# Performance work log

Hardware: AMD Instinct MI355X
Metric: run time of the kernel (lower is better)

The kernel has to match this reference:

```python
import jax, jax.numpy as jnp
import numpy as np
from jax import lax

DIM = 256
HEADS = 8
SR = 4
EPS = 1e-5
SCALE = (DIM // HEADS) ** -0.5


def _dwconv(x, wgt, stride, pad):
    # x: (B,C,H,W), wgt: (C,1,kh,kw) depthwise
    return lax.conv_general_dilated(
        x, wgt, (stride, stride), [(pad, pad), (pad, pad)],
        feature_group_count=x.shape[1],
        dimension_numbers=("NCHW", "OIHW", "NCHW"))


def _bn(x, g, b, m, v):
    # eval-mode batchnorm folded to per-channel scale/shift
    s = g / jnp.sqrt(v + EPS)
    return x * s[:, None, None] + (b - m * s)[:, None, None]


def setup_inputs() -> dict:
    key = jax.random.key(0)
    ks = jax.random.split(key, 16)
    b, h, w = 8, 64, 64
    c = DIM
    n = h * w

    def rn(k, shape, s=0.05):
        return jax.random.normal(k, shape, jnp.float32) * s

    return dict(
        x=jax.random.normal(ks[0], (b, n, c), jnp.float32),
        h=h, w=w,
        Wq=rn(ks[1], (c, c)), bq=rn(ks[2], (c,)),
        Wkv=rn(ks[3], (2 * c, c)), bkv=rn(ks[4], (2 * c,)),
        sr_w1=rn(ks[5], (c, 1, SR + 3, SR + 3), 0.1),
        bn1_gamma=1.0 + rn(ks[6], (c,)), bn1_beta=rn(ks[7], (c,)),
        bn1_mean=rn(ks[8], (c,)), bn1_var=jnp.abs(1.0 + rn(ks[9], (c,))),
        sr_w2=1.0 + rn(ks[10], (c,), 0.2),  # 1x1 depthwise conv == per-channel scale
        bn2_gamma=1.0 + rn(ks[11], (c,)), bn2_beta=rn(ks[12], (c,)),
        bn2_mean=rn(ks[13], (c,)), bn2_var=jnp.abs(1.0 + rn(ks[14], (c,))),
        local_w=rn(ks[15], (c, 1, 3, 3), 0.1),
        local_b=jnp.zeros((c,), jnp.float32),
    )


def reference(x, h, w, Wq, bq, Wkv, bkv, sr_w1, bn1_gamma, bn1_beta, bn1_mean,
              bn1_var, sr_w2, bn2_gamma, bn2_beta, bn2_mean, bn2_var,
              local_w, local_b):
    b, n, c = x.shape
    hd = c // HEADS
    xi = x.transpose(0, 2, 1).reshape(b, c, h, w)  # (b,c,h,w)

    # q projection (1x1 conv == channel matmul)
    q = jnp.einsum("bchw,dc->bdhw", xi, Wq) + bq[None, :, None, None]
    q = q.reshape(b, HEADS, hd, n).transpose(0, 1, 3, 2)  # (b,H,n,hd)

    # spatial reduction: dwconv7 s4 + BN + GELU + dw1x1 + BN
    kv = _dwconv(xi, sr_w1, SR, (SR + 3) // 2)
    kv = _bn(kv, bn1_gamma, bn1_beta, bn1_mean, bn1_var)
    kv = jax.nn.gelu(kv, approximate=False)
    kv = kv * sr_w2[None, :, None, None]
    kv = _bn(kv, bn2_gamma, bn2_beta, bn2_mean, bn2_var)

    # residual local depthwise 3x3 conv
    kv = _dwconv(kv, local_w, 1, 1) + local_b[None, :, None, None] + kv

    # kv projection and split
    kvp = jnp.einsum("bchw,dc->bdhw", kv, Wkv) + bkv[None, :, None, None]
    k_, v_ = jnp.split(kvp, 2, axis=1)
    m = k_.shape[2] * k_.shape[3]
    k_ = k_.reshape(b, HEADS, hd, m)                       # (b,H,hd,m)
    v_ = v_.reshape(b, HEADS, hd, m).transpose(0, 1, 3, 2)  # (b,H,m,hd)

    attn = jax.nn.softmax(jnp.einsum("bhnd,bhdm->bhnm", q, k_) * SCALE, axis=-1)
    out = jnp.einsum("bhnm,bhmd->bhnd", attn, v_)           # (b,H,n,hd)
    out = out.transpose(0, 1, 3, 2).reshape(b, c, n).transpose(0, 2, 1)
    return out
```

## Files before the change

kernel.cpp:

```cpp
#include <hip/hip_runtime.h>
#include <math.h>

typedef __bf16 bf16;
typedef bf16 bf16x4 __attribute__((ext_vector_type(4)));
typedef bf16 bf16x8 __attribute__((ext_vector_type(8)));
typedef float f32x4 __attribute__((ext_vector_type(4)));

static_assert(sizeof(bf16x8) == 16, "bf16x8 must be 16B");

#define QSCALE (0.17677669529663687f * 1.4426950408889634f)

__device__ __forceinline__ f32x4 mfma16(bf16x8 a, bf16x8 b, f32x4 c) {
  return __builtin_amdgcn_mfma_f32_16x16x32_bf16(a, b, c, 0, 0, 0);
}

__global__ __launch_bounds__(256) void k_cvt(
    const float* __restrict__ Wq, const float* __restrict__ Wkv,
    const float* __restrict__ w7, bf16* __restrict__ Wqb,
    bf16* __restrict__ Wkvb, float* __restrict__ w7t) {
  const int tid = threadIdx.x;
  const int blk = blockIdx.x;
  if (blk < 96) {
    const float* src;
    bf16* dst;
    if (blk < 32) {
      const int idx = blk * 256 + tid;
      src = Wq + (size_t)idx * 8;
      dst = Wqb + (size_t)idx * 8;
    } else {
      const int idx = (blk - 32) * 256 + tid;
      src = Wkv + (size_t)idx * 8;
      dst = Wkvb + (size_t)idx * 8;
    }
    const float4 a = ((const float4*)src)[0];
    const float4 b = ((const float4*)src)[1];
    bf16x8 r;
    r[0] = (bf16)a.x; r[1] = (bf16)a.y; r[2] = (bf16)a.z; r[3] = (bf16)a.w;
    r[4] = (bf16)b.x; r[5] = (bf16)b.y; r[6] = (bf16)b.z; r[7] = (bf16)b.w;
    *(bf16x8*)dst = r;
  } else {
    const int c = tid;
    #pragma unroll
    for (int tap = 0; tap < 49; tap++)
      w7t[tap * 256 + c] = w7[c * 49 + tap];
  }
}

__global__ __launch_bounds__(256) void k_sr(
    const float* __restrict__ x, const float* __restrict__ w7t,
    const float* __restrict__ g1, const float* __restrict__ b1,
    const float* __restrict__ m1, const float* __restrict__ v1,
    const float* __restrict__ sw2,
    const float* __restrict__ g2, const float* __restrict__ b2,
    const float* __restrict__ m2, const float* __restrict__ v2,
    bf16* __restrict__ kv1) {
  __shared__ float part[4][256];
  const int tid = threadIdx.x;
  const int team = tid >> 6, g = tid & 63;
  const int c0 = g * 4;
  const int blk = blockIdx.x;
  const int b = blk & 7, m = blk >> 3;
  const int oy = m >> 4, ox = m & 15;

  float4 xv[13], wv[13];
  float msk[13];
  #pragma unroll
  for (int j = 0; j < 13; j++) {
    const int tap = team + j * 4;
    const int ky = tap / 7, kx = tap - ky * 7;
    const int iy = oy * 4 - 3 + ky, ix = ox * 4 - 3 + kx;
    msk[j] = (tap < 49 && iy >= 0 && iy < 64 && ix >= 0 && ix < 64) ? 1.f : 0.f;
    const int iyc = iy < 0 ? 0 : (iy > 63 ? 63 : iy);
    const int ixc = ix < 0 ? 0 : (ix > 63 ? 63 : ix);
    const int tc = tap > 48 ? 48 : tap;
    xv[j] = *(const float4*)(x + ((size_t)b * 4096 + iyc * 64 + ixc) * 256 + c0);
    wv[j] = *(const float4*)(w7t + tc * 256 + c0);
  }
  float a0 = 0.f, a1 = 0.f, a2 = 0.f, a3 = 0.f;
  #pragma unroll
  for (int j = 0; j < 13; j++) {
    a0 += xv[j].x * wv[j].x * msk[j];
    a1 += xv[j].y * wv[j].y * msk[j];
    a2 += xv[j].z * wv[j].z * msk[j];
    a3 += xv[j].w * wv[j].w * msk[j];
  }
  *(f32x4*)&part[team][c0] = (f32x4){a0, a1, a2, a3};
  __syncthreads();
  const int c = tid;
  float y = part[0][c] + part[1][c] + part[2][c] + part[3][c];
  float s = g1[c] / sqrtf(v1[c] + 1e-5f);
  y = y * s + (b1[c] - m1[c] * s);
  y = 0.5f * y * (1.f + erff(y * 0.70710678118654752f));
  y *= sw2[c];
  s = g2[c] / sqrtf(v2[c] + 1e-5f);
  y = y * s + (b2[c] - m2[c] * s);
  kv1[((size_t)b * 256 + m) * 256 + c] = (bf16)y;
}

__global__ __launch_bounds__(256) void k_localkv(
    const bf16* __restrict__ kv1, const float* __restrict__ w3,
    const float* __restrict__ lb, const bf16* __restrict__ Wkvb,
    const float* __restrict__ bkv, bf16* __restrict__ k_a,
    bf16* __restrict__ v_b) {
  __shared__ bf16 halo[3][10][256];
  __shared__ float rows[8][256];
  const int c = threadIdx.x;
  const int mt = blockIdx.x;
  const int b = blockIdx.y;
  const int oy = mt >> 1, o0 = (mt & 1) * 8;

  #pragma unroll
  for (int p = 0; p < 30; p++) {
    const int dy = p / 10, xi = p - dy * 10;
    const int iy = oy - 1 + dy, ix = o0 - 1 + xi;
    const bool ok = (iy >= 0 && iy < 16 && ix >= 0 && ix < 16);
    const int iyc = ok ? iy : 0, ixc = ok ? ix : 0;
    const bf16 v = kv1[((size_t)b * 256 + iyc * 16 + ixc) * 256 + c];
    halo[dy][xi][c] = ok ? v : (bf16)0.f;
  }
  float w3f[9];
  #pragma unroll
  for (int t = 0; t < 9; t++) w3f[t] = w3[c * 9 + t];
  const float lbf = lb[c];
  __syncthreads();

  #pragma unroll
  for (int r = 0; r < 8; r++) {
    float acc = lbf + (float)halo[1][r + 1][c];
    #pragma unroll
    for (int ky = 0; ky < 3; ky++)
      #pragma unroll
      for (int kx = 0; kx < 3; kx++)
        acc += (float)halo[ky][r + kx][c] * w3f[ky * 3 + kx];
    rows[r][c] = acc;
  }
  __syncthreads();

  const int tid = c;
  float acck[8] = {0}, accv[8] = {0};
  for (int oc = 0; oc < 32; oc++) {
    const bf16x8 w0 = *(const bf16x8*)(Wkvb + (size_t)tid * 256 + oc * 8);
    const bf16x8 w1 = *(const bf16x8*)(Wkvb + ((size_t)tid + 256) * 256 + oc * 8);
    float wf0[8], wf1[8];
    #pragma unroll
    for (int j = 0; j < 8; j++) { wf0[j] = (float)w0[j]; wf1[j] = (float)w1[j]; }
    #pragma unroll
    for (int r = 0; r < 8; r++) {
      const float4* rp = (const float4*)&rows[r][oc * 8];
      const float4 ra = rp[0], rb = rp[1];
      const float rv[8] = {ra.x, ra.y, ra.z, ra.w, rb.x, rb.y, rb.z, rb.w};
      #pragma unroll
      for (int j = 0; j < 8; j++) {
        acck[r] += wf0[j] * rv[j];
        accv[r] += wf1[j] * rv[j];
      }
    }
  }
  const float bk = bkv[tid], bv = bkv[tid + 256];
  const int h = tid >> 5, d = tid & 31;
  #pragma unroll
  for (int r = 0; r < 8; r++) {
    const int m = (oy * 16 + o0) + r;
    k_a[(((size_t)b * 8 + h) * 256 + m) * 32 + d] = (bf16)(acck[r] + bk);
    v_b[(((size_t)b * 8 + h) * 32 + d) * 256 + m] = (bf16)(accv[r] + bv);
  }
}

__global__ __launch_bounds__(256) void k_qattn(
    const float* __restrict__ x, const bf16* __restrict__ Wqb,
    const float* __restrict__ bq, const bf16* __restrict__ k_a,
    const bf16* __restrict__ v_b, float* __restrict__ out) {
  __shared__ bf16 qx[64 * 264];
  const int tid = threadIdx.x, wv = tid >> 6, lane = tid & 63;
  const int qd = lane >> 4, l15 = lane & 15;
  const int b = blockIdx.y;
  const int n0 = blockIdx.x * 64;

  #pragma unroll
  for (int it = 0; it < 8; it++) {
    const int idx = it * 256 + tid;
    const int lr = idx >> 5, pos = idx & 31;
    const float* src = x + ((size_t)b * 4096 + n0 + lr) * 256 + pos * 8;
    const float4 a = ((const float4*)src)[0];
    const float4 bb = ((const float4*)src)[1];
    bf16x8 r;
    r[0] = (bf16)a.x;  r[1] = (bf16)a.y;  r[2] = (bf16)a.z;  r[3] = (bf16)a.w;
    r[4] = (bf16)bb.x; r[5] = (bf16)bb.y; r[6] = (bf16)bb.z; r[7] = (bf16)bb.w;
    *(bf16x8*)(qx + lr * 264 + pos * 8) = r;
  }
  __syncthreads();

  bf16x8 af[8];
  #pragma unroll
  for (int kc = 0; kc < 8; kc++)
    af[kc] = *(const bf16x8*)(qx + (wv * 16 + l15) * 264 + kc * 32 + qd * 8);

  f32x4 acc[16];
  #pragma unroll
  for (int dt = 0; dt < 16; dt++) acc[dt] = (f32x4){0.f, 0.f, 0.f, 0.f};
  #pragma unroll
  for (int dt = 0; dt < 16; dt++) {
    #pragma unroll
    for (int kc = 0; kc < 8; kc++) {
      const bf16x8 bb =
          *(const bf16x8*)(Wqb + (size_t)(dt * 16 + l15) * 256 + kc * 32 + qd * 8);
      acc[dt] = mfma16(af[kc], bb, acc[dt]);
    }
  }
  #pragma unroll
  for (int dt = 0; dt < 16; dt++) {
    const int d = dt * 16 + l15;
    const float bias = bq[d];
    #pragma unroll
    for (int r = 0; r < 4; r++) {
      const int row = wv * 16 + qd * 4 + r;
      qx[row * 264 + d] = (bf16)((acc[dt][r] + bias) * QSCALE);
    }
  }

  const bf16* kb = k_a + (size_t)(b * 8) * 256 * 32;
  const bf16* vb = v_b + (size_t)(b * 8) * 32 * 256;
  const int kperm = 8 * (l15 >> 2) + (l15 & 3);
  const int nn = n0 + wv * 16 + l15;
  float* ob = out + ((size_t)b * 4096 + nn) * 256;

  for (int h = 0; h < 8; h++) {
    const bf16* kh = kb + (size_t)h * 256 * 32;
    const bf16* vh = vb + (size_t)h * 32 * 256;
    const bf16x8 qf =
        *(const bf16x8*)(qx + (wv * 16 + l15) * 264 + h * 32 + qd * 8);
    f32x4 a0 = (f32x4){0.f, 0.f, 0.f, 0.f};
    f32x4 a1 = (f32x4){0.f, 0.f, 0.f, 0.f};
    float lr = 0.f;
    #pragma unroll
    for (int ch = 0; ch < 8; ch++) {
      const bf16x8 ka0 =
          *(const bf16x8*)(kh + (size_t)(ch * 32 + kperm) * 32 + qd * 8);
      const bf16x8 ka1 =
          *(const bf16x8*)(kh + (size_t)(ch * 32 + kperm + 4) * 32 + qd * 8);
      const bf16x8 va0 =
          *(const bf16x8*)(vh + (size_t)l15 * 256 + ch * 32 + qd * 8);
      const bf16x8 va1 =
          *(const bf16x8*)(vh + (size_t)(16 + l15) * 256 + ch * 32 + qd * 8);
      const f32x4 z = (f32x4){0.f, 0.f, 0.f, 0.f};
      f32x4 s0 = mfma16(ka0, qf, z);
      f32x4 s1 = mfma16(ka1, qf, z);
      float p[8];
      #pragma unroll
      for (int j = 0; j < 4; j++) {
        p[j] = __builtin_amdgcn_exp2f(fminf(s0[j], 80.f));
        p[4 + j] = __builtin_amdgcn_exp2f(fminf(s1[j], 80.f));
      }
      bf16x8 pb;
      #pragma unroll
      for (int j = 0; j < 8; j++) { lr += p[j]; pb[j] = (bf16)p[j]; }
      a0 = mfma16(va0, pb, a0);
      a1 = mfma16(va1, pb, a1);
    }
    lr += __shfl_xor(lr, 16, 64);
    lr += __shfl_xor(lr, 32, 64);
    const float inv = 1.f / lr;
    *(float4*)(ob + h * 32 + qd * 4) =
        (float4){a0[0] * inv, a0[1] * inv, a0[2] * inv, a0[3] * inv};
    *(float4*)(ob + h * 32 + 16 + qd * 4) =
        (float4){a1[0] * inv, a1[1] * inv, a1[2] * inv, a1[3] * inv};
  }
}

extern "C" void kernel_launch(void* const* d_in, const int* in_sizes, int n_in,
                              void* d_out, int out_size, void* d_ws, size_t ws_size,
                              hipStream_t stream) {
  const float* x      = (const float*)d_in[0];
  const float* Wq     = (const float*)d_in[3];
  const float* bq     = (const float*)d_in[4];
  const float* Wkv    = (const float*)d_in[5];
  const float* bkv    = (const float*)d_in[6];
  const float* sr_w1  = (const float*)d_in[7];
  const float* bn1_g  = (const float*)d_in[8];
  const float* bn1_b  = (const float*)d_in[9];
  const float* bn1_m  = (const float*)d_in[10];
  const float* bn1_v  = (const float*)d_in[11];
  const float* sw2    = (const float*)d_in[12];
  const float* bn2_g  = (const float*)d_in[13];
  const float* bn2_b  = (const float*)d_in[14];
  const float* bn2_m  = (const float*)d_in[15];
  const float* bn2_v  = (const float*)d_in[16];
  const float* lw     = (const float*)d_in[17];
  const float* lb     = (const float*)d_in[18];

  const int B = in_sizes[0] / (4096 * 256);

  bf16* Wqb  = (bf16*)d_ws;
  bf16* Wkvb = Wqb + 65536;
  float* w7t = (float*)(Wkvb + 131072);
  bf16* kv1  = (bf16*)(w7t + 12544);
  bf16* k_a  = kv1 + (size_t)B * 256 * 256;
  bf16* v_b  = k_a + (size_t)B * 8 * 256 * 32;

  k_cvt<<<dim3(97), 256, 0, stream>>>(Wq, Wkv, sr_w1, Wqb, Wkvb, w7t);
  k_sr<<<dim3(256 * B), 256, 0, stream>>>(x, w7t, bn1_g, bn1_b, bn1_m, bn1_v,
                                          sw2, bn2_g, bn2_b, bn2_m, bn2_v, kv1);
  k_localkv<<<dim3(32, B), 256, 0, stream>>>(kv1, lw, lb, Wkvb, bkv, k_a, v_b);
  k_qattn<<<dim3(64, B), 256, 0, stream>>>(x, Wqb, bq, k_a, v_b, (float*)d_out);
}
```

Before: 229.3 us.

## Split attention across head-pair blocks, one head per wave with K/V prefetch

The q-attention kernel now launches twice as many blocks, each handling four heads. Each wave owns one head and processes all 64 query rows, so every K/V fragment it loads is reused across four query tiles, and the next chunk's K/V is prefetched in registers. The cost is that the Q projection (x load plus the full 256x256 matmul) is done twice per query tile, once in each head-half block, and register pressure rises from the extra accumulators. Barriers were added around the shared-memory reuse of qx, which is needed now that waves read rows written by other waves.

```diff
diff --git a/kernel.cpp b/kernel.cpp
--- a/kernel.cpp
+++ b/kernel.cpp
@@ -173,7 +173,7 @@
   __shared__ bf16 qx[64 * 264];
   const int tid = threadIdx.x, wv = tid >> 6, lane = tid & 63;
   const int qd = lane >> 4, l15 = lane & 15;
-  const int b = blockIdx.y;
+  const int b = blockIdx.z;
   const int n0 = blockIdx.x * 64;
 
   #pragma unroll
@@ -207,6 +207,7 @@
       acc[dt] = mfma16(af[kc], bb, acc[dt]);
     }
   }
+  __syncthreads();
   #pragma unroll
   for (int dt = 0; dt < 16; dt++) {
     const int d = dt * 16 + l15;
@@ -217,53 +218,74 @@
       qx[row * 264 + d] = (bf16)((acc[dt][r] + bias) * QSCALE);
     }
   }
-
-  const bf16* kb = k_a + (size_t)(b * 8) * 256 * 32;
-  const bf16* vb = v_b + (size_t)(b * 8) * 32 * 256;
+  __syncthreads();
+
+  const int h = blockIdx.y * 4 + wv;
+  const int bh = b * 8 + h;
+  const bf16* kb = k_a + (size_t)bh * 256 * 32;
+  const bf16* vb = v_b + (size_t)bh * 32 * 256;
+
+  bf16x8 qf[4];
+  #pragma unroll
+  for (int qi = 0; qi < 4; qi++)
+    qf[qi] = *(const bf16x8*)(qx + (qi * 16 + l15) * 264 + h * 32 + qd * 8);
+
+  f32x4 oacc[4][2];
+  float lr[4] = {0.f, 0.f, 0.f, 0.f};
+  #pragma unroll
+  for (int qi = 0; qi < 4; qi++) {
+    oacc[qi][0] = (f32x4){0.f, 0.f, 0.f, 0.f};
+    oacc[qi][1] = (f32x4){0.f, 0.f, 0.f, 0.f};
+  }
   const int kperm = 8 * (l15 >> 2) + (l15 & 3);
-  const int nn = n0 + wv * 16 + l15;
-  float* ob = out + ((size_t)b * 4096 + nn) * 256;
-
-  for (int h = 0; h < 8; h++) {
-    const bf16* kh = kb + (size_t)h * 256 * 32;
-    const bf16* vh = vb + (size_t)h * 32 * 256;
-    const bf16x8 qf =
-        *(const bf16x8*)(qx + (wv * 16 + l15) * 264 + h * 32 + qd * 8);
-    f32x4 a0 = (f32x4){0.f, 0.f, 0.f, 0.f};
-    f32x4 a1 = (f32x4){0.f, 0.f, 0.f, 0.f};
-    float lr = 0.f;
-    #pragma unroll
-    for (int ch = 0; ch < 8; ch++) {
-      const bf16x8 ka0 =
-          *(const bf16x8*)(kh + (size_t)(ch * 32 + kperm) * 32 + qd * 8);
-      const bf16x8 ka1 =
-          *(const bf16x8*)(kh + (size_t)(ch * 32 + kperm + 4) * 32 + qd * 8);
-      const bf16x8 va0 =
-          *(const bf16x8*)(vh + (size_t)l15 * 256 + ch * 32 + qd * 8);
-      const bf16x8 va1 =
-          *(const bf16x8*)(vh + (size_t)(16 + l15) * 256 + ch * 32 + qd * 8);
-      const f32x4 z = (f32x4){0.f, 0.f, 0.f, 0.f};
-      f32x4 s0 = mfma16(ka0, qf, z);
-      f32x4 s1 = mfma16(ka1, qf, z);
-      float p[8];
+
+  bf16x8 ka0 = *(const bf16x8*)(kb + (size_t)kperm * 32 + qd * 8);
+  bf16x8 ka1 = *(const bf16x8*)(kb + (size_t)(kperm + 4) * 32 + qd * 8);
+  bf16x8 va0 = *(const bf16x8*)(vb + (size_t)l15 * 256 + qd * 8);
+  bf16x8 va1 = *(const bf16x8*)(vb + (size_t)(16 + l15) * 256 + qd * 8);
+
+  for (int ch = 0; ch < 8; ch++) {
+    const int cn = (ch < 7 ? ch + 1 : 7) * 32;
+    const bf16x8 nk0 = *(const bf16x8*)(kb + (size_t)(cn + kperm) * 32 + qd * 8);
+    const bf16x8 nk1 = *(const bf16x8*)(kb + (size_t)(cn + kperm + 4) * 32 + qd * 8);
+    const bf16x8 nv0 = *(const bf16x8*)(vb + (size_t)l15 * 256 + cn + qd * 8);
+    const bf16x8 nv1 = *(const bf16x8*)(vb + (size_t)(16 + l15) * 256 + cn + qd * 8);
+    const f32x4 z = (f32x4){0.f, 0.f, 0.f, 0.f};
+    #pragma unroll
+    for (int qi = 0; qi < 4; qi++) {
+      f32x4 s0 = mfma16(ka0, qf[qi], z);
+      f32x4 s1 = mfma16(ka1, qf[qi], z);
+      float p[8], ls = 0.f;
       #pragma unroll
       for (int j = 0; j < 4; j++) {
         p[j] = __builtin_amdgcn_exp2f(fminf(s0[j], 80.f));
         p[4 + j] = __builtin_amdgcn_exp2f(fminf(s1[j], 80.f));
       }
+      #pragma unroll
+      for (int j = 0; j < 8; j++) ls += p[j];
+      lr[qi] += ls;
       bf16x8 pb;
       #pragma unroll
-      for (int j = 0; j < 8; j++) { lr += p[j]; pb[j] = (bf16)p[j]; }
-      a0 = mfma16(va0, pb, a0);
-      a1 = mfma16(va1, pb, a1);
-    }
-    lr += __shfl_xor(lr, 16, 64);
-    lr += __shfl_xor(lr, 32, 64);
-    const float inv = 1.f / lr;
-    *(float4*)(ob + h * 32 + qd * 4) =
-        (float4){a0[0] * inv, a0[1] * inv, a0[2] * inv, a0[3] * inv};
-    *(float4*)(ob + h * 32 + 16 + qd * 4) =
-        (float4){a1[0] * inv, a1[1] * inv, a1[2] * inv, a1[3] * inv};
+      for (int j = 0; j < 8; j++) pb[j] = (bf16)p[j];
+      oacc[qi][0] = mfma16(va0, pb, oacc[qi][0]);
+      oacc[qi][1] = mfma16(va1, pb, oacc[qi][1]);
+    }
+    ka0 = nk0; ka1 = nk1; va0 = nv0; va1 = nv1;
+  }
+  #pragma unroll
+  for (int qi = 0; qi < 4; qi++) {
+    float l = lr[qi];
+    l += __shfl_xor(l, 16, 64);
+    l += __shfl_xor(l, 32, 64);
+    const float inv = 1.f / l;
+    const int nn = n0 + qi * 16 + l15;
+    float* ob = out + (size_t)(b * 4096 + nn) * 256 + h * 32;
+    #pragma unroll
+    for (int t = 0; t < 2; t++) {
+      *(float4*)(ob + t * 16 + qd * 4) =
+          (float4){oacc[qi][t][0] * inv, oacc[qi][t][1] * inv,
+                   oacc[qi][t][2] * inv, oacc[qi][t][3] * inv};
+    }
   }
 }
 
@@ -301,5 +323,6 @@
   k_sr<<<dim3(256 * B), 256, 0, stream>>>(x, w7t, bn1_g, bn1_b, bn1_m, bn1_v,
                                           sw2, bn2_g, bn2_b, bn2_m, bn2_v, kv1);
   k_localkv<<<dim3(32, B), 256, 0, stream>>>(kv1, lw, lb, Wkvb, bkv, k_a, v_b);
-  k_qattn<<<dim3(64, B), 256, 0, stream>>>(x, Wqb, bq, k_a, v_b, (float*)d_out);
-}
+  k_qattn<<<dim3(64, 2, B), 256, 0, stream>>>(x, Wqb, bq, k_a, v_b,
+                                              (float*)d_out);
+}
```

After: 237.6 us. +3.6%, slower.
